# Performance work log

Measured on AMD Instinct MI355X. Metric: run time of the kernel, lower is better.

Reference implementation:

```python
import jax, jax.numpy as jnp
import numpy as np

N_ATOMS, N_NBH, N_IN, N_FILTERS, N_OUT, N_GAUSS = 10000, 48, 128, 128, 128, 25
R_CUTOFF = 5.0
LOG2 = float(np.log(2.0))


def ssp(v):
    # shifted softplus, the SchNet activation
    return jax.nn.softplus(v) - LOG2


def setup_inputs() -> dict:
    key = jax.random.key(0)
    ks = jax.random.split(key, 10)
    x = jax.random.normal(ks[0], (N_ATOMS, N_IN), dtype=jnp.float32)
    dR = jax.random.uniform(ks[1], (N_ATOMS, N_NBH), dtype=jnp.float32) * 10.0  # distances in [0,10)
    dR_expanded = jax.random.normal(ks[2], (N_ATOMS, N_NBH, N_GAUSS), dtype=jnp.float32)
    pairwise_mask = jnp.ones((N_ATOMS, N_NBH), dtype=jnp.float32)
    neighbors_idx = jax.random.randint(ks[3], (N_ATOMS, N_NBH), 0, N_ATOMS, dtype=jnp.int32)
    s = 1.0 / np.sqrt(N_FILTERS)
    W1 = jax.random.normal(ks[4], (N_GAUSS, N_FILTERS), dtype=jnp.float32) * (1.0 / np.sqrt(N_GAUSS))
    b1 = jnp.zeros((N_FILTERS,), dtype=jnp.float32)
    W2 = jax.random.normal(ks[5], (N_FILTERS, N_FILTERS), dtype=jnp.float32) * s
    b2 = jnp.zeros((N_FILTERS,), dtype=jnp.float32)
    W_in2f = jax.random.normal(ks[6], (N_IN, N_FILTERS), dtype=jnp.float32) * (1.0 / np.sqrt(N_IN))
    W_f2out = jax.random.normal(ks[7], (N_FILTERS, N_OUT), dtype=jnp.float32) * s
    b_f2out = jnp.zeros((N_OUT,), dtype=jnp.float32)
    return {"x": x, "dR": dR, "dR_expanded": dR_expanded, "pairwise_mask": pairwise_mask,
            "neighbors_idx": neighbors_idx, "W1": W1, "b1": b1, "W2": W2, "b2": b2,
            "W_in2f": W_in2f, "W_f2out": W_f2out, "b_f2out": b_f2out}


def reference(x, dR, dR_expanded, pairwise_mask, neighbors_idx,
              W1, b1, W2, b2, W_in2f, W_f2out, b_f2out):
    # FilterNetwork: Dense + ssp + Dense, on Gaussian-smeared distances -> [N, K, F]
    W = jnp.einsum('nkg,gf->nkf', dR_expanded, W1) + b1
    W = jnp.einsum('nkf,fh->nkh', ssp(W), W2) + b2
    # HardCutoff: 1 where within cutoff
    C = (dR <= R_CUTOFF).astype(W.dtype)           # [N, K]
    W = W * C[..., None]
    # in2f (no bias), gather neighbor features
    y = x @ W_in2f                                  # [N, F]
    y = jnp.take(y, neighbors_idx, axis=0)          # [N, K, F] (gather == take_along_axis path)
    # filter-weighted multiply + masked sum aggregation over neighbor axis
    y = y * W
    y = jnp.sum(y * pairwise_mask[..., None], axis=1)  # [N, F]
    # f2out: Linear + shifted softplus
    return ssp(y @ W_f2out + b_f2out)               # [N, n_out]
```

## Files before the change

### kernel.cpp

```cpp
#include <hip/hip_runtime.h>
#include <hip/hip_bf16.h>


#define NA 10000
#define NK 48
#define NF 128
#define HP  136
#define YFP 136

typedef __bf16 bf16x8 __attribute__((ext_vector_type(8)));
typedef float  f32x4  __attribute__((ext_vector_type(4)));

__device__ __forceinline__ unsigned short f2bs(float x) {
    return __builtin_bit_cast(unsigned short, (__bf16)x);
}
__device__ __forceinline__ float bs2f(unsigned short u) {
    return (float)__builtin_bit_cast(__bf16, u);
}
__device__ __forceinline__ float sspf(float v) {
    return fmaxf(v, 0.0f) + __logf(1.0f + __expf(-fabsf(v))) - 0.69314718056f;
}

__global__ __launch_bounds__(256) void in2f_prep(
    const float* __restrict__ x,
    const float* __restrict__ Wi,
    const float* __restrict__ W1,
    const float* __restrict__ W2,
    const float* __restrict__ Wo,
    unsigned short* __restrict__ wsb,
    unsigned short* __restrict__ yfeatb)
{
    const int tid = threadIdx.x;

    if (blockIdx.x >= 157) {
        int i = (blockIdx.x - 157) * 256 + tid;
        if (i < 4096) {
            int f = i >> 5, g = i & 31;
            wsb[i] = (g < 25) ? f2bs(W1[g * NF + f]) : (unsigned short)0;
        } else if (i < 20480) {
            int j = i - 4096; int h = j >> 7, k = j & 127;
            wsb[i] = f2bs(W2[k * NF + h]);
        } else {
            int j = i - 20480; int f = j >> 7, k = j & 127;
            wsb[i] = f2bs(Wo[k * NF + f]);
        }
        return;
    }

    __shared__ __align__(16) unsigned short s_wi[NF * 136];
    {
        const float4* wi4 = (const float4*)Wi;
        #pragma unroll
        for (int it = 0; it < 16; ++it) {
            int idx4 = it * 256 + tid;
            float4 v = wi4[idx4];
            int i = idx4 >> 5;
            int f = (idx4 & 31) * 4;
            s_wi[(f + 0) * 136 + i] = f2bs(v.x);
            s_wi[(f + 1) * 136 + i] = f2bs(v.y);
            s_wi[(f + 2) * 136 + i] = f2bs(v.z);
            s_wi[(f + 3) * 136 + i] = f2bs(v.w);
        }
    }
    __syncthreads();

    const int w = tid >> 6;
    const int lane = tid & 63;
    const int r = lane & 15;
    const int q = lane >> 4;
    const int m0 = blockIdx.x * 64 + w * 16;
    const int row = m0 + r;
    const bool rv = (row < NA);

    f32x4 acc[8];
    #pragma unroll
    for (int nt = 0; nt < 8; ++nt) { acc[nt][0]=0.f; acc[nt][1]=0.f; acc[nt][2]=0.f; acc[nt][3]=0.f; }

    #pragma unroll
    for (int ks = 0; ks < 4; ++ks) {
        bf16x8 a;
        if (rv) {
            const float4* xp = (const float4*)(x + (size_t)row * NF + ks * 32 + q * 8);
            float4 v0 = xp[0], v1 = xp[1];
            a[0]=(__bf16)v0.x; a[1]=(__bf16)v0.y; a[2]=(__bf16)v0.z; a[3]=(__bf16)v0.w;
            a[4]=(__bf16)v1.x; a[5]=(__bf16)v1.y; a[6]=(__bf16)v1.z; a[7]=(__bf16)v1.w;
        } else {
            #pragma unroll
            for (int j = 0; j < 8; ++j) a[j] = (__bf16)0.0f;
        }
        #pragma unroll
        for (int nt = 0; nt < 8; ++nt) {
            bf16x8 b = *(const bf16x8*)(&s_wi[(nt * 16 + r) * 136 + ks * 32 + q * 8]);
            acc[nt] = __builtin_amdgcn_mfma_f32_16x16x32_bf16(a, b, acc[nt], 0, 0, 0);
        }
    }
    #pragma unroll
    for (int nt = 0; nt < 8; ++nt) {
        #pragma unroll
        for (int reg = 0; reg < 4; ++reg) {
            int orow = m0 + q * 4 + reg;
            if (orow < NA)
                yfeatb[(size_t)orow * NF + nt * 16 + r] = f2bs(acc[nt][reg]);
        }
    }
}

__global__ __launch_bounds__(256) void cfconv_p(
    const float* __restrict__ dR,
    const float* __restrict__ dRe,
    const float* __restrict__ mask,
    const int*   __restrict__ nbr,
    const float* __restrict__ b1,
    const float* __restrict__ b2,
    const unsigned short* __restrict__ W1T,
    const unsigned short* __restrict__ W2T,
    const unsigned short* __restrict__ yfeatb,
    float* __restrict__ yout)
{
    __shared__ __align__(16) unsigned short s_H[NK * HP];
    __shared__ __align__(16) unsigned short s_yf[NK * YFP];
    __shared__ float s_cm[NK];

    const int tid = threadIdx.x;
    const int w = tid >> 6;
    const int lane = tid & 63;
    const int r = lane & 15;
    const int q = lane >> 4;
    const int nt0 = w * 2;
    const int kb = tid >> 4;
    const int sp = tid & 15;

    bf16x8 bfr0 = *(const bf16x8*)(W1T + ((nt0    ) * 16 + r) * 32 + q * 8);
    bf16x8 bfr1 = *(const bf16x8*)(W1T + ((nt0 + 1) * 16 + r) * 32 + q * 8);
    bf16x8 bw[2][4];
    #pragma unroll
    for (int t = 0; t < 2; ++t)
        #pragma unroll
        for (int ks = 0; ks < 4; ++ks)
            bw[t][ks] = *(const bf16x8*)(W2T + ((nt0 + t) * 16 + r) * NF + ks * 32 + q * 8);
    const float bias1a = b1[nt0 * 16 + r];
    const float bias1b = b1[nt0 * 16 + 16 + r];
    const float bias2a = b2[nt0 * 16 + r];
    const float bias2b = b2[nt0 * 16 + 16 + r];

    for (int n = blockIdx.x; n < NA; n += gridDim.x) {
        const int nb0 = nbr[n * NK + kb] * NF;
        const int nb1 = nbr[n * NK + kb + 16] * NF;
        const int nb2 = nbr[n * NK + kb + 32] * NF;
        bf16x8 g0 = *(const bf16x8*)(yfeatb + nb0 + sp * 8);
        bf16x8 g1 = *(const bf16x8*)(yfeatb + nb1 + sp * 8);
        bf16x8 g2 = *(const bf16x8*)(yfeatb + nb2 + sp * 8);

        if (tid < NK) {
            float d = dR[n * NK + tid];
            float m = mask[n * NK + tid];
            s_cm[tid] = (d <= 5.0f) ? m : 0.0f;
        }

        const float* dre_n = dRe + (size_t)n * (NK * 25);
        #pragma unroll
        for (int mt = 0; mt < 3; ++mt) {
            bf16x8 av8;
            if (q < 3) {
                float av[8];
                __builtin_memcpy(av, dre_n + (mt * 16 + r) * 25 + q * 8, 32);
                #pragma unroll
                for (int j = 0; j < 8; ++j) av8[j] = (__bf16)av[j];
            } else {
                float v = dre_n[(mt * 16 + r) * 25 + 24];
                av8[0] = (__bf16)v;
                #pragma unroll
                for (int j = 1; j < 8; ++j) av8[j] = (__bf16)0.0f;
            }
            f32x4 zf; zf[0]=0.f; zf[1]=0.f; zf[2]=0.f; zf[3]=0.f;
            f32x4 h0v = __builtin_amdgcn_mfma_f32_16x16x32_bf16(av8, bfr0, zf, 0, 0, 0);
            f32x4 h1v = __builtin_amdgcn_mfma_f32_16x16x32_bf16(av8, bfr1, zf, 0, 0, 0);
            #pragma unroll
            for (int reg = 0; reg < 4; ++reg) {
                int k = mt * 16 + q * 4 + reg;
                s_H[k * HP + nt0 * 16 + r]      = f2bs(sspf(h0v[reg] + bias1a));
                s_H[k * HP + nt0 * 16 + 16 + r] = f2bs(sspf(h1v[reg] + bias1b));
            }
        }

        *(bf16x8*)(&s_yf[(kb     ) * YFP + sp * 8]) = g0;
        *(bf16x8*)(&s_yf[(kb + 16) * YFP + sp * 8]) = g1;
        *(bf16x8*)(&s_yf[(kb + 32) * YFP + sp * 8]) = g2;

        __syncthreads();

        f32x4 acc[3][2];
        #pragma unroll
        for (int mt = 0; mt < 3; ++mt)
            #pragma unroll
            for (int t = 0; t < 2; ++t) { acc[mt][t][0]=0.f; acc[mt][t][1]=0.f; acc[mt][t][2]=0.f; acc[mt][t][3]=0.f; }

        #pragma unroll
        for (int ks = 0; ks < 4; ++ks) {
            #pragma unroll
            for (int mt = 0; mt < 3; ++mt) {
                bf16x8 ah = *(const bf16x8*)(&s_H[(mt * 16 + r) * HP + ks * 32 + q * 8]);
                acc[mt][0] = __builtin_amdgcn_mfma_f32_16x16x32_bf16(ah, bw[0][ks], acc[mt][0], 0, 0, 0);
                acc[mt][1] = __builtin_amdgcn_mfma_f32_16x16x32_bf16(ah, bw[1][ks], acc[mt][1], 0, 0, 0);
            }
        }

        float part0 = 0.f, part1 = 0.f;
        const int h0 = nt0 * 16 + r;
        #pragma unroll
        for (int mt = 0; mt < 3; ++mt) {
            #pragma unroll
            for (int reg = 0; reg < 4; ++reg) {
                int k = mt * 16 + q * 4 + reg;
                float cmk = s_cm[k];
                part0 += cmk * (acc[mt][0][reg] + bias2a) * bs2f(s_yf[k * YFP + h0]);
                part1 += cmk * (acc[mt][1][reg] + bias2b) * bs2f(s_yf[k * YFP + h0 + 16]);
            }
        }
        part0 += __shfl_xor(part0, 16);
        part0 += __shfl_xor(part0, 32);
        part1 += __shfl_xor(part1, 16);
        part1 += __shfl_xor(part1, 32);
        if (q == 0) {
            yout[(size_t)n * NF + h0]      = part0;
            yout[(size_t)n * NF + h0 + 16] = part1;
        }

        __syncthreads();
    }
}

__global__ __launch_bounds__(256) void f2out_mfma(
    const unsigned short* __restrict__ WoT,
    const float* __restrict__ bo,
    float* io)
{
    const int tid = threadIdx.x;
    const int w = tid >> 6;
    const int lane = tid & 63;
    const int r = lane & 15;
    const int q = lane >> 4;
    const int m0 = blockIdx.x * 64 + w * 16;
    const int row = m0 + r;
    const bool rv = (row < NA);

    f32x4 acc[8];
    #pragma unroll
    for (int nt = 0; nt < 8; ++nt) { acc[nt][0]=0.f; acc[nt][1]=0.f; acc[nt][2]=0.f; acc[nt][3]=0.f; }

    #pragma unroll
    for (int ks = 0; ks < 4; ++ks) {
        bf16x8 a;
        if (rv) {
            const float4* yp = (const float4*)(io + (size_t)row * NF + ks * 32 + q * 8);
            float4 v0 = yp[0], v1 = yp[1];
            a[0]=(__bf16)v0.x; a[1]=(__bf16)v0.y; a[2]=(__bf16)v0.z; a[3]=(__bf16)v0.w;
            a[4]=(__bf16)v1.x; a[5]=(__bf16)v1.y; a[6]=(__bf16)v1.z; a[7]=(__bf16)v1.w;
        } else {
            #pragma unroll
            for (int j = 0; j < 8; ++j) a[j] = (__bf16)0.0f;
        }
        #pragma unroll
        for (int nt = 0; nt < 8; ++nt) {
            bf16x8 b = *(const bf16x8*)(WoT + (nt * 16 + r) * NF + ks * 32 + q * 8);
            acc[nt] = __builtin_amdgcn_mfma_f32_16x16x32_bf16(a, b, acc[nt], 0, 0, 0);
        }
    }
    #pragma unroll
    for (int nt = 0; nt < 8; ++nt) {
        float bia = bo[nt * 16 + r];
        #pragma unroll
        for (int reg = 0; reg < 4; ++reg) {
            int orow = m0 + q * 4 + reg;
            if (orow < NA)
                io[(size_t)orow * NF + nt * 16 + r] = sspf(acc[nt][reg] + bia);
        }
    }
}

extern "C" void kernel_launch(void* const* d_in, const int* in_sizes, int n_in,
                              void* d_out, int out_size, void* d_ws, size_t ws_size,
                              hipStream_t stream)
{
    const float* x    = (const float*)d_in[0];
    const float* dR   = (const float*)d_in[1];
    const float* dRe  = (const float*)d_in[2];
    const float* mask = (const float*)d_in[3];
    const int*   nbr  = (const int*)d_in[4];
    const float* W1   = (const float*)d_in[5];
    const float* b1   = (const float*)d_in[6];
    const float* W2   = (const float*)d_in[7];
    const float* b2   = (const float*)d_in[8];
    const float* Wi2f = (const float*)d_in[9];
    const float* Wf2o = (const float*)d_in[10];
    const float* bf2o = (const float*)d_in[11];
    float* out = (float*)d_out;

    unsigned short* wsb = (unsigned short*)d_ws;
    unsigned short* W1T    = wsb;
    unsigned short* W2T    = wsb + 4096;
    unsigned short* WoT    = wsb + 20480;
    unsigned short* yfeatb = wsb + 36864;

    in2f_prep<<<301, 256, 0, stream>>>(x, Wi2f, W1, W2, Wf2o, wsb, yfeatb);
    cfconv_p<<<1250, 256, 0, stream>>>(dR, dRe, mask, nbr, b1, b2,
                                       W1T, W2T, yfeatb, out);
    f2out_mfma<<<157, 256, 0, stream>>>(WoT, bf2o, out);
}
```

Before: 202.5 us.

## Pre-convert dR_expanded to padded bf16 and software-pipeline cfconv atom loop

Adds a prep stage that converts dR_expanded from fp32 into a bf16 buffer padded to 32 per neighbor, so the cfconv kernel can do aligned 16-byte loads instead of unaligned fp32 loads plus conversion. The cfconv loop is restructured to prefetch the next atom's gathers, filter inputs and cutoff data, and to compute its first-layer filter MFMA while the current atom's second GEMM and reduction run. The grid shrinks to 1024 persistent blocks with a launch-bounds occupancy hint. The extra pass rereads the full dR_expanded tensor and writes a bf16 copy, which costs bandwidth and raises register pressure from the held prefetch state.

```diff
diff --git a/kernel.cpp b/kernel.cpp
--- a/kernel.cpp
+++ b/kernel.cpp
@@ -7,6 +7,7 @@
 #define NF 128
 #define HP  136
 #define YFP 136
+#define GRID_CF 1024
 
 typedef __bf16 bf16x8 __attribute__((ext_vector_type(8)));
 typedef float  f32x4  __attribute__((ext_vector_type(4)));
@@ -27,10 +28,36 @@
     const float* __restrict__ W1,
     const float* __restrict__ W2,
     const float* __restrict__ Wo,
+    const float* __restrict__ dRe,
     unsigned short* __restrict__ wsb,
-    unsigned short* __restrict__ yfeatb)
+    unsigned short* __restrict__ yfeatb,
+    unsigned short* __restrict__ dreb)
 {
     const int tid = threadIdx.x;
+
+    if (blockIdx.x >= 301) {
+        const float4* src = (const float4*)dRe;
+        for (int j = (blockIdx.x - 301) * 256 + tid; j < 3000000; j += 768 * 256) {
+            float4 v = src[j];
+            int n  = j / 300;
+            int rm = j - n * 300;
+            int i  = rm * 4;
+            int k  = i / 25;
+            int g  = i - k * 25;
+            unsigned short* dst = dreb + (size_t)n * 1536;
+            float vv[4] = {v.x, v.y, v.z, v.w};
+            #pragma unroll
+            for (int e = 0; e < 4; ++e) {
+                dst[k * 32 + g] = f2bs(vv[e]);
+                if (++g == 25) {
+                    #pragma unroll
+                    for (int p = 25; p < 32; ++p) dst[k * 32 + p] = 0;
+                    g = 0; ++k;
+                }
+            }
+        }
+        return;
+    }
 
     if (blockIdx.x >= 157) {
         int i = (blockIdx.x - 157) * 256 + tid;
@@ -105,15 +132,15 @@
     }
 }
 
-__global__ __launch_bounds__(256) void cfconv_p(
+__global__ __launch_bounds__(256, 4) void cfconv_pp(
     const float* __restrict__ dR,
-    const float* __restrict__ dRe,
     const float* __restrict__ mask,
     const int*   __restrict__ nbr,
     const float* __restrict__ b1,
     const float* __restrict__ b2,
     const unsigned short* __restrict__ W1T,
     const unsigned short* __restrict__ W2T,
+    const unsigned short* __restrict__ dreb,
     const unsigned short* __restrict__ yfeatb,
     float* __restrict__ yout)
 {
@@ -130,8 +157,8 @@
     const int kb = tid >> 4;
     const int sp = tid & 15;
 
-    bf16x8 bfr0 = *(const bf16x8*)(W1T + ((nt0    ) * 16 + r) * 32 + q * 8);
-    bf16x8 bfr1 = *(const bf16x8*)(W1T + ((nt0 + 1) * 16 + r) * 32 + q * 8);
+    const bf16x8 bfr0 = *(const bf16x8*)(W1T + ((nt0    ) * 16 + r) * 32 + q * 8);
+    const bf16x8 bfr1 = *(const bf16x8*)(W1T + ((nt0 + 1) * 16 + r) * 32 + q * 8);
     bf16x8 bw[2][4];
     #pragma unroll
     for (int t = 0; t < 2; ++t)
@@ -143,51 +170,71 @@
     const float bias2a = b2[nt0 * 16 + r];
     const float bias2b = b2[nt0 * 16 + 16 + r];
 
-    for (int n = blockIdx.x; n < NA; n += gridDim.x) {
-        const int nb0 = nbr[n * NK + kb] * NF;
-        const int nb1 = nbr[n * NK + kb + 16] * NF;
-        const int nb2 = nbr[n * NK + kb + 32] * NF;
-        bf16x8 g0 = *(const bf16x8*)(yfeatb + nb0 + sp * 8);
-        bf16x8 g1 = *(const bf16x8*)(yfeatb + nb1 + sp * 8);
-        bf16x8 g2 = *(const bf16x8*)(yfeatb + nb2 + sp * 8);
-
+    bf16x8 g0, g1, g2;
+    bf16x8 a0, a1, a2;
+    float dv = 10.0f, mv = 0.0f;
+    unsigned short hsv[24];
+
+    auto prefetch = [&](int nn) {
+        const int nb0 = nbr[nn * NK + kb] * NF;
+        const int nb1 = nbr[nn * NK + kb + 16] * NF;
+        const int nb2 = nbr[nn * NK + kb + 32] * NF;
+        g0 = *(const bf16x8*)(yfeatb + nb0 + sp * 8);
+        g1 = *(const bf16x8*)(yfeatb + nb1 + sp * 8);
+        g2 = *(const bf16x8*)(yfeatb + nb2 + sp * 8);
+        const unsigned short* dn = dreb + (size_t)nn * 1536;
+        a0 = *(const bf16x8*)(dn + (     r) * 32 + q * 8);
+        a1 = *(const bf16x8*)(dn + (16 + r) * 32 + q * 8);
+        a2 = *(const bf16x8*)(dn + (32 + r) * 32 + q * 8);
         if (tid < NK) {
-            float d = dR[n * NK + tid];
-            float m = mask[n * NK + tid];
-            s_cm[tid] = (d <= 5.0f) ? m : 0.0f;
-        }
-
-        const float* dre_n = dRe + (size_t)n * (NK * 25);
+            dv = dR[nn * NK + tid];
+            mv = mask[nn * NK + tid];
+        }
+    };
+
+    auto stage1 = [&]() {
         #pragma unroll
         for (int mt = 0; mt < 3; ++mt) {
-            bf16x8 av8;
-            if (q < 3) {
-                float av[8];
-                __builtin_memcpy(av, dre_n + (mt * 16 + r) * 25 + q * 8, 32);
-                #pragma unroll
-                for (int j = 0; j < 8; ++j) av8[j] = (__bf16)av[j];
-            } else {
-                float v = dre_n[(mt * 16 + r) * 25 + 24];
-                av8[0] = (__bf16)v;
-                #pragma unroll
-                for (int j = 1; j < 8; ++j) av8[j] = (__bf16)0.0f;
-            }
+            bf16x8 av8 = (mt == 0) ? a0 : (mt == 1) ? a1 : a2;
             f32x4 zf; zf[0]=0.f; zf[1]=0.f; zf[2]=0.f; zf[3]=0.f;
             f32x4 h0v = __builtin_amdgcn_mfma_f32_16x16x32_bf16(av8, bfr0, zf, 0, 0, 0);
             f32x4 h1v = __builtin_amdgcn_mfma_f32_16x16x32_bf16(av8, bfr1, zf, 0, 0, 0);
             #pragma unroll
             for (int reg = 0; reg < 4; ++reg) {
+                hsv[mt * 8 + reg]     = f2bs(sspf(h0v[reg] + bias1a));
+                hsv[mt * 8 + 4 + reg] = f2bs(sspf(h1v[reg] + bias1b));
+            }
+        }
+    };
+
+    auto ldswrite = [&]() {
+        #pragma unroll
+        for (int mt = 0; mt < 3; ++mt) {
+            #pragma unroll
+            for (int reg = 0; reg < 4; ++reg) {
                 int k = mt * 16 + q * 4 + reg;
-                s_H[k * HP + nt0 * 16 + r]      = f2bs(sspf(h0v[reg] + bias1a));
-                s_H[k * HP + nt0 * 16 + 16 + r] = f2bs(sspf(h1v[reg] + bias1b));
-            }
-        }
-
+                s_H[k * HP + nt0 * 16 + r]      = hsv[mt * 8 + reg];
+                s_H[k * HP + nt0 * 16 + 16 + r] = hsv[mt * 8 + 4 + reg];
+            }
+        }
         *(bf16x8*)(&s_yf[(kb     ) * YFP + sp * 8]) = g0;
         *(bf16x8*)(&s_yf[(kb + 16) * YFP + sp * 8]) = g1;
         *(bf16x8*)(&s_yf[(kb + 32) * YFP + sp * 8]) = g2;
-
-        __syncthreads();
+        if (tid < NK)
+            s_cm[tid] = (dv <= 5.0f) ? mv : 0.0f;
+    };
+
+    int n = blockIdx.x;
+    prefetch(n);
+    stage1();
+    ldswrite();
+    __syncthreads();
+
+    while (true) {
+        const int n_next = n + GRID_CF;
+        const bool more = (n_next < NA);
+
+        if (more) prefetch(n_next);
 
         f32x4 acc[3][2];
         #pragma unroll
@@ -204,6 +251,8 @@
                 acc[mt][1] = __builtin_amdgcn_mfma_f32_16x16x32_bf16(ah, bw[1][ks], acc[mt][1], 0, 0, 0);
             }
         }
+
+        if (more) stage1();
 
         float part0 = 0.f, part1 = 0.f;
         const int h0 = nt0 * 16 + r;
@@ -226,7 +275,12 @@
             yout[(size_t)n * NF + h0 + 16] = part1;
         }
 
+        if (!more) break;
+
         __syncthreads();
+        ldswrite();
+        __syncthreads();
+        n = n_next;
     }
 }
 
@@ -301,9 +355,11 @@
     unsigned short* W2T    = wsb + 4096;
     unsigned short* WoT    = wsb + 20480;
     unsigned short* yfeatb = wsb + 36864;
-
-    in2f_prep<<<301, 256, 0, stream>>>(x, Wi2f, W1, W2, Wf2o, wsb, yfeatb);
-    cfconv_p<<<1250, 256, 0, stream>>>(dR, dRe, mask, nbr, b1, b2,
-                                       W1T, W2T, yfeatb, out);
+    unsigned short* dreb   = wsb + 1316864;
+
+    in2f_prep<<<1069, 256, 0, stream>>>(x, Wi2f, W1, W2, Wf2o, dRe,
+                                        wsb, yfeatb, dreb);
+    cfconv_pp<<<GRID_CF, 256, 0, stream>>>(dR, mask, nbr, b1, b2,
+                                           W1T, W2T, dreb, yfeatb, out);
     f2out_mfma<<<157, 256, 0, stream>>>(WoT, bf2o, out);
 }
```

Result: slower. 209.5 us (+3.4%).
